# Optimization experiments

Hardware: AMD Instinct MI355X
Metric: run time of the kernel (lower is better)

The kernel has to match this reference:

```python
import jax, jax.numpy as jnp
import numpy as np

B, H, Q_TOK, D = 8, 12, 577, 64
N_SIDE = 24  # 24x24 = 576 patches, +1 CLS row/col -> 577


def _pairwise_dists():
    rows, cols = np.indices((N_SIDE, N_SIDE))
    idx = np.stack([rows.flatten(), cols.flatten()], axis=-1).astype(np.float32)  # (576, 2)
    d = idx[:, None, :] - idx[None, :, :]  # (576, 576, 2)
    d = np.pad(d, ((1, 0), (1, 0), (0, 0)))  # zero-pad CLS token row/col -> (577, 577, 2)
    return jnp.asarray(d)


def setup_inputs() -> dict:
    key = jax.random.key(0)
    ks = jax.random.split(key, 4)
    query = jax.random.normal(ks[0], (B, H, Q_TOK, D), jnp.float32)
    W1 = jax.random.normal(ks[1], (D, 64), jnp.float32) * 0.05
    b1 = jnp.zeros((64,), jnp.float32)
    W2 = jax.random.normal(ks[2], (64, 3), jnp.float32) * 0.05
    b2 = jnp.zeros((3,), jnp.float32)
    # uniform noise for RelaxedBernoulli reparameterized sample
    u = jax.random.uniform(ks[3], (B, H, Q_TOK, Q_TOK), jnp.float32, 1e-6, 1.0 - 1e-6)
    temperature = jnp.ones((1,), jnp.float32)
    return {"query": query, "W1": W1, "b1": b1, "W2": W2, "b2": b2,
            "dists": _pairwise_dists(), "u": u, "temperature": temperature}


def reference(query, W1, b1, W2, b2, dists, u, temperature):
    # sigma MLP: Linear -> exact GELU -> Linear, per (b,h,q) token
    hdn = jax.nn.gelu(query @ W1 + b1, approximate=False)
    sig = hdn @ W2 + b2  # (b,h,q,3)
    sy = jnp.exp(sig[..., 0]) + 1.0
    sx = jnp.exp(sig[..., 1]) + 1.0
    rho = jnp.tanh(sig[..., 2]) * 0.99
    cov = sy * sx * rho
    # 2x2 covariance matrix per query: [[sy^2, sy*sx*rho],[sy*sx*rho, sx^2]]
    Sigma = jnp.stack([jnp.stack([sy * sy, cov], -1),
                       jnp.stack([cov, sx * sx], -1)], -2)  # (b,h,q,2,2)
    # closed-form 2x2 inverse (same math as torch.linalg.inv)
    det = (sy * sx) ** 2 * (1.0 - rho * rho)
    inv00 = (sx * sx) / det
    inv11 = (sy * sy) / det
    inv01 = -cov / det
    dy = dists[..., 0]  # (q,k)
    dx = dists[..., 1]
    # Mahalanobis quadratic form, fused (no (b,h,q,k,2,2) intermediates)
    quad = (inv00[..., None] * (dy * dy)
            + 2.0 * inv01[..., None] * (dy * dx)
            + inv11[..., None] * (dx * dx))  # (b,h,q,k)
    kernel = jnp.exp(-0.5 * quad)
    probs = kernel / jnp.max(kernel, axis=-1, keepdims=True)
    probs = jnp.minimum(probs, 1.0)
    # RelaxedBernoulli rsample: sigmoid((logit(p) + logistic_noise) / T)
    logits = jnp.log(probs) - jnp.log1p(-probs)
    noise = jnp.log(u) - jnp.log1p(-u)
    mask = jax.nn.sigmoid((logits + noise) / temperature[0])
    return mask, Sigma
```

## Files before the change

kernel.cpp:

```cpp
#include <hip/hip_runtime.h>
#include <math.h>

constexpr int BB = 8, HH = 12, QT = 577, DD = 64;
constexpr int NTOK = BB * HH * QT;
constexpr long long MASK_ELEMS = (long long)NTOK * QT;
constexpr int NBH = BB * HH;
constexpr int WAVES_PER_BLOCK = 8;
constexpr int CHUNKS = NBH / WAVES_PER_BLOCK;

using f4 = __attribute__((ext_vector_type(4))) float;

__global__ __launch_bounds__(256)
void mlp_sigma(const float* __restrict__ query,
               const float* __restrict__ W1,
               const float* __restrict__ b1,
               const float* __restrict__ W2,
               const float* __restrict__ b2,
               f4* __restrict__ Sig)
{
    const int token = (blockIdx.x * 256 + threadIdx.x) >> 6;
    const int lane  = threadIdx.x & 63;
    if (token >= NTOK) return;

    const float qv = query[(size_t)token * DD + lane];
    float acc = b1[lane];
#pragma unroll
    for (int i = 0; i < DD; ++i)
        acc = fmaf(__shfl(qv, i), W1[i * DD + lane], acc);
    const float h = 0.5f * acc * (1.0f + erff(acc * 0.7071067811865476f));

    float p0 = h * W2[lane * 3 + 0];
    float p1 = h * W2[lane * 3 + 1];
    float p2 = h * W2[lane * 3 + 2];
#pragma unroll
    for (int off = 32; off > 0; off >>= 1) {
        p0 += __shfl_xor(p0, off);
        p1 += __shfl_xor(p1, off);
        p2 += __shfl_xor(p2, off);
    }
    if (lane == 0) {
        const float sy  = expf(p0 + b2[0]) + 1.0f;
        const float sx  = expf(p1 + b2[1]) + 1.0f;
        const float rho = tanhf(p2 + b2[2]) * 0.99f;
        const float cov = sy * sx * rho;
        f4 s; s.x = sy * sy; s.y = cov; s.z = cov; s.w = sx * sx;
        Sig[token] = s;
    }
}

template<bool T1>
__device__ __forceinline__ float mask_elem(float g0, float g1, float g2,
                                           float j0, float j1, float j2,
                                           float uv, float invT)
{
    const float hq = fmaxf(fmaf(j2, g2, fmaf(j1, g1, j0 * g0)), 0.0f);
    const float E  = __expf(hq);
    const float a  = E - 1.0f;
    if (T1)
        return __fdividef(uv, fmaf(a, 1.0f - uv, uv));
    const float rr = __fdividef(a * (1.0f - uv), uv);
    return __fdividef(1.0f, 1.0f + __expf(__logf(rr) * invT));
}

template<bool T1>
__device__ __forceinline__ void do_row(const f4* __restrict__ G4,
                                       const float* __restrict__ up,
                                       float* __restrict__ mp,
                                       const float* __restrict__ u,
                                       float* __restrict__ out,
                                       unsigned base, int h, int NV,
                                       const int* bc, int lane,
                                       float j0, float j1, float j2, float invT)
{
#pragma unroll
    for (int p = 0; p < 3; ++p) {
        const int idx = p * 64 + lane;
        if (idx < NV) {
            const f4 uu = *(const f4*)(up + 4 * idx);
            f4 m4;
#pragma unroll
            for (int c = 0; c < 4; ++c) {
                const f4 g = G4[bc[c] + idx];
                m4[c] = mask_elem<T1>(g.x, g.y, g.z, j0, j1, j2, uu[c], invT);
            }
            __builtin_nontemporal_store(m4, (f4*)(mp + 4 * idx));
        }
    }
    const int scnt = QT - 4 * NV;
    if (lane < scnt) {
        const int k = (lane < h) ? lane : (h + 4 * NV + (lane - h));
        const f4 g = G4[(k & 3) * 160 + (k >> 2)];
        const float m = mask_elem<T1>(g.x, g.y, g.z, j0, j1, j2,
                                      u[base + k], invT);
        __builtin_nontemporal_store(m, out + base + k);
    }
}

__global__ __launch_bounds__(512)
void mask_hyb(const float* __restrict__ u,
              const float* __restrict__ temp,
              float* __restrict__ out)
{
    __shared__ f4 G4[640];

    const f4* __restrict__ Sig = (const f4*)(out + MASK_ELEMS);
    const int q     = blockIdx.x;
    const int chunk = blockIdx.y;
    const int wave  = threadIdx.x >> 6;
    const int lane  = threadIdx.x & 63;

    const int token = (chunk * WAVES_PER_BLOCK + wave) * QT + q;
    const f4 S = Sig[token];
    const float tval = temp[0];

    const unsigned base = (unsigned)token * (unsigned)QT;
    const int h  = (int)((0u - base) & 3u);
    const int NV = (QT - h) >> 2;
    const float* __restrict__ up = u   + base + h;
    float*       __restrict__ mp = out + base + h;
    int bc[4];
#pragma unroll
    for (int c = 0; c < 4; ++c)
        bc[c] = ((h + c) & 3) * 160 + ((h + c) >> 2);

    {
        const int qm1 = (q > 0) ? q - 1 : 0;
        const int qr  = (int)((unsigned)qm1 / 24u);
        const int qc  = qm1 - qr * 24;
        const float fqr = (float)qr, fqc = (float)qc;
        const bool qz = (q == 0);
        for (int k = threadIdx.x; k < QT; k += 512) {
            const int km1 = (k > 0) ? k - 1 : 0;
            const int kr  = (int)((unsigned)km1 / 24u);
            const int kc  = km1 - kr * 24;
            float dy = fqr - (float)kr;
            float dx = fqc - (float)kc;
            if (qz | (k == 0)) { dy = 0.0f; dx = 0.0f; }
            f4 g; g.x = dy * dy; g.y = dy * dx; g.z = dx * dx; g.w = 0.0f;
            G4[(k & 3) * 160 + (k >> 2)] = g;
        }
    }
    __syncthreads();

    const float rdet = __fdividef(1.0f, fmaf(S.x, S.w, -S.y * S.y));
    const float j0 =  0.5f * S.w * rdet;
    const float j1 = -S.y * rdet;
    const float j2 =  0.5f * S.x * rdet;

    const float invT = __int_as_float(__builtin_amdgcn_readfirstlane(
                           __float_as_int(__fdividef(1.0f, tval))));
    if (invT == 1.0f)
        do_row<true >(G4, up, mp, u, out, base, h, NV, bc, lane, j0, j1, j2, invT);
    else
        do_row<false>(G4, up, mp, u, out, base, h, NV, bc, lane, j0, j1, j2, invT);
}

extern "C" void kernel_launch(void* const* d_in, const int* in_sizes, int n_in,
                              void* d_out, int out_size, void* d_ws, size_t ws_size,
                              hipStream_t stream) {
    const float* query = (const float*)d_in[0];
    const float* W1    = (const float*)d_in[1];
    const float* b1    = (const float*)d_in[2];
    const float* W2    = (const float*)d_in[3];
    const float* b2    = (const float*)d_in[4];
    const float* u     = (const float*)d_in[6];
    const float* temp  = (const float*)d_in[7];
    float* out = (float*)d_out;

    f4* Sig = (f4*)(out + MASK_ELEMS);
    mlp_sigma<<<dim3(NTOK / 4), dim3(256), 0, stream>>>(query, W1, b1, W2, b2, Sig);
    mask_hyb<<<dim3(QT, CHUNKS), dim3(512), 0, stream>>>(u, temp, out);
}
```

Measured before the change: 303.2 us.

## Fuse sigma MLP into mask kernel and prefetch u row before compute

Removes the separate MLP kernel and computes each token's sigma inside the mask kernel: W1 is staged in shared memory per block and each wave runs the 64x64 MLP for its own query token. The u row loads are issued up front so their latency overlaps the MLP and the distance-table setup. This drops one launch and the Sigma round-trip through global memory. In exchange, every block reloads W1 (16KB) into LDS, which raises shared-memory use and could lower occupancy.

```diff
diff --git a/kernel.cpp b/kernel.cpp
--- a/kernel.cpp
+++ b/kernel.cpp
@@ -9,44 +9,6 @@
 constexpr int CHUNKS = NBH / WAVES_PER_BLOCK;
 
 using f4 = __attribute__((ext_vector_type(4))) float;
-
-__global__ __launch_bounds__(256)
-void mlp_sigma(const float* __restrict__ query,
-               const float* __restrict__ W1,
-               const float* __restrict__ b1,
-               const float* __restrict__ W2,
-               const float* __restrict__ b2,
-               f4* __restrict__ Sig)
-{
-    const int token = (blockIdx.x * 256 + threadIdx.x) >> 6;
-    const int lane  = threadIdx.x & 63;
-    if (token >= NTOK) return;
-
-    const float qv = query[(size_t)token * DD + lane];
-    float acc = b1[lane];
-#pragma unroll
-    for (int i = 0; i < DD; ++i)
-        acc = fmaf(__shfl(qv, i), W1[i * DD + lane], acc);
-    const float h = 0.5f * acc * (1.0f + erff(acc * 0.7071067811865476f));
-
-    float p0 = h * W2[lane * 3 + 0];
-    float p1 = h * W2[lane * 3 + 1];
-    float p2 = h * W2[lane * 3 + 2];
-#pragma unroll
-    for (int off = 32; off > 0; off >>= 1) {
-        p0 += __shfl_xor(p0, off);
-        p1 += __shfl_xor(p1, off);
-        p2 += __shfl_xor(p2, off);
-    }
-    if (lane == 0) {
-        const float sy  = expf(p0 + b2[0]) + 1.0f;
-        const float sx  = expf(p1 + b2[1]) + 1.0f;
-        const float rho = tanhf(p2 + b2[2]) * 0.99f;
-        const float cov = sy * sx * rho;
-        f4 s; s.x = sy * sy; s.y = cov; s.z = cov; s.w = sx * sx;
-        Sig[token] = s;
-    }
-}
 
 template<bool T1>
 __device__ __forceinline__ float mask_elem(float g0, float g1, float g2,
@@ -63,65 +25,62 @@
 }
 
 template<bool T1>
-__device__ __forceinline__ void do_row(const f4* __restrict__ G4,
-                                       const float* __restrict__ up,
-                                       float* __restrict__ mp,
-                                       const float* __restrict__ u,
-                                       float* __restrict__ out,
-                                       unsigned base, int h, int NV,
-                                       const int* bc, int lane,
-                                       float j0, float j1, float j2, float invT)
+__device__ __forceinline__ void do_pass(const f4* __restrict__ G4,
+                                        const int* bc, int idx, f4 uu,
+                                        float* __restrict__ mp,
+                                        float j0, float j1, float j2, float invT)
 {
+    f4 m4;
 #pragma unroll
-    for (int p = 0; p < 3; ++p) {
-        const int idx = p * 64 + lane;
-        if (idx < NV) {
-            const f4 uu = *(const f4*)(up + 4 * idx);
-            f4 m4;
-#pragma unroll
-            for (int c = 0; c < 4; ++c) {
-                const f4 g = G4[bc[c] + idx];
-                m4[c] = mask_elem<T1>(g.x, g.y, g.z, j0, j1, j2, uu[c], invT);
-            }
-            __builtin_nontemporal_store(m4, (f4*)(mp + 4 * idx));
-        }
+    for (int c = 0; c < 4; ++c) {
+        const f4 g = G4[bc[c] + idx];
+        m4[c] = mask_elem<T1>(g.x, g.y, g.z, j0, j1, j2, uu[c], invT);
     }
-    const int scnt = QT - 4 * NV;
-    if (lane < scnt) {
-        const int k = (lane < h) ? lane : (h + 4 * NV + (lane - h));
-        const f4 g = G4[(k & 3) * 160 + (k >> 2)];
-        const float m = mask_elem<T1>(g.x, g.y, g.z, j0, j1, j2,
-                                      u[base + k], invT);
-        __builtin_nontemporal_store(m, out + base + k);
-    }
+    __builtin_nontemporal_store(m4, (f4*)(mp + 4 * idx));
 }
 
-__global__ __launch_bounds__(512)
-void mask_hyb(const float* __restrict__ u,
-              const float* __restrict__ temp,
-              float* __restrict__ out)
+__global__ __launch_bounds__(512, 6)
+void fused_mask(const float* __restrict__ query,
+                const float* __restrict__ W1,
+                const float* __restrict__ b1,
+                const float* __restrict__ W2,
+                const float* __restrict__ b2,
+                const float* __restrict__ u,
+                const float* __restrict__ temp,
+                float* __restrict__ out)
 {
-    __shared__ f4 G4[640];
+    __shared__ f4    G4[640];
+    __shared__ float W1s[DD * DD];
 
-    const f4* __restrict__ Sig = (const f4*)(out + MASK_ELEMS);
+    f4* __restrict__ SigOut = (f4*)(out + MASK_ELEMS);
     const int q     = blockIdx.x;
     const int chunk = blockIdx.y;
-    const int wave  = threadIdx.x >> 6;
-    const int lane  = threadIdx.x & 63;
+    const int tid   = threadIdx.x;
+    const int wave  = tid >> 6, lane = tid & 63;
 
     const int token = (chunk * WAVES_PER_BLOCK + wave) * QT + q;
-    const f4 S = Sig[token];
-    const float tval = temp[0];
-
     const unsigned base = (unsigned)token * (unsigned)QT;
     const int h  = (int)((0u - base) & 3u);
     const int NV = (QT - h) >> 2;
     const float* __restrict__ up = u   + base + h;
     float*       __restrict__ mp = out + base + h;
-    int bc[4];
-#pragma unroll
-    for (int c = 0; c < 4; ++c)
-        bc[c] = ((h + c) & 3) * 160 + ((h + c) >> 2);
+
+    const f4 uu0 = *(const f4*)(up + 4 * lane);
+    const f4 uu1 = *(const f4*)(up + 4 * (64 + lane));
+    const int idx2 = 128 + lane;
+    f4 uu2 = {};
+    if (idx2 < NV) uu2 = *(const f4*)(up + 4 * idx2);
+    const int scnt = QT - 4 * NV;
+    int ks = 0; float us = 0.0f;
+    if (lane < scnt) {
+        ks = (lane < h) ? lane : (h + 4 * NV + (lane - h));
+        us = u[base + ks];
+    }
+    const float tval = temp[0];
+    const float qv   = query[(size_t)token * DD + lane];
+
+    ((f4*)W1s)[tid]       = ((const f4*)W1)[tid];
+    ((f4*)W1s)[tid + 512] = ((const f4*)W1)[tid + 512];
 
     {
         const int qm1 = (q > 0) ? q - 1 : 0;
@@ -129,7 +88,7 @@
         const int qc  = qm1 - qr * 24;
         const float fqr = (float)qr, fqc = (float)qc;
         const bool qz = (q == 0);
-        for (int k = threadIdx.x; k < QT; k += 512) {
+        for (int k = tid; k < QT; k += 512) {
             const int km1 = (k > 0) ? k - 1 : 0;
             const int kr  = (int)((unsigned)km1 / 24u);
             const int kc  = km1 - kr * 24;
@@ -142,17 +101,64 @@
     }
     __syncthreads();
 
-    const float rdet = __fdividef(1.0f, fmaf(S.x, S.w, -S.y * S.y));
-    const float j0 =  0.5f * S.w * rdet;
-    const float j1 = -S.y * rdet;
-    const float j2 =  0.5f * S.x * rdet;
+    float acc = b1[lane];
+#pragma unroll
+    for (int i = 0; i < DD; ++i)
+        acc = fmaf(__shfl(qv, i), W1s[i * DD + lane], acc);
+    const float hg = 0.5f * acc * (1.0f + erff(acc * 0.7071067811865476f));
+
+    float p0 = hg * W2[lane * 3 + 0];
+    float p1 = hg * W2[lane * 3 + 1];
+    float p2 = hg * W2[lane * 3 + 2];
+#pragma unroll
+    for (int off = 32; off > 0; off >>= 1) {
+        p0 += __shfl_xor(p0, off);
+        p1 += __shfl_xor(p1, off);
+        p2 += __shfl_xor(p2, off);
+    }
+    const float sy  = expf(p0 + b2[0]) + 1.0f;
+    const float sx  = expf(p1 + b2[1]) + 1.0f;
+    const float rho = tanhf(p2 + b2[2]) * 0.99f;
+    const float cov = sy * sx * rho;
+    const float Sx = sy * sy, Sw = sx * sx, Sy = cov;
+    if (lane == 0) {
+        f4 s; s.x = Sx; s.y = Sy; s.z = Sy; s.w = Sw;
+        SigOut[token] = s;
+    }
+
+    const float rdet = __fdividef(1.0f, fmaf(Sx, Sw, -Sy * Sy));
+    const float j0 =  0.5f * Sw * rdet;
+    const float j1 = -Sy * rdet;
+    const float j2 =  0.5f * Sx * rdet;
+
+    int bc[4];
+#pragma unroll
+    for (int c = 0; c < 4; ++c)
+        bc[c] = ((h + c) & 3) * 160 + ((h + c) >> 2);
 
     const float invT = __int_as_float(__builtin_amdgcn_readfirstlane(
                            __float_as_int(__fdividef(1.0f, tval))));
-    if (invT == 1.0f)
-        do_row<true >(G4, up, mp, u, out, base, h, NV, bc, lane, j0, j1, j2, invT);
-    else
-        do_row<false>(G4, up, mp, u, out, base, h, NV, bc, lane, j0, j1, j2, invT);
+    if (invT == 1.0f) {
+        do_pass<true >(G4, bc, lane,      uu0, mp, j0, j1, j2, invT);
+        do_pass<true >(G4, bc, 64 + lane, uu1, mp, j0, j1, j2, invT);
+        if (idx2 < NV)
+            do_pass<true >(G4, bc, idx2,  uu2, mp, j0, j1, j2, invT);
+        if (lane < scnt) {
+            const f4 g = G4[(ks & 3) * 160 + (ks >> 2)];
+            const float m = mask_elem<true >(g.x, g.y, g.z, j0, j1, j2, us, invT);
+            __builtin_nontemporal_store(m, out + base + ks);
+        }
+    } else {
+        do_pass<false>(G4, bc, lane,      uu0, mp, j0, j1, j2, invT);
+        do_pass<false>(G4, bc, 64 + lane, uu1, mp, j0, j1, j2, invT);
+        if (idx2 < NV)
+            do_pass<false>(G4, bc, idx2,  uu2, mp, j0, j1, j2, invT);
+        if (lane < scnt) {
+            const f4 g = G4[(ks & 3) * 160 + (ks >> 2)];
+            const float m = mask_elem<false>(g.x, g.y, g.z, j0, j1, j2, us, invT);
+            __builtin_nontemporal_store(m, out + base + ks);
+        }
+    }
 }
 
 extern "C" void kernel_launch(void* const* d_in, const int* in_sizes, int n_in,
@@ -167,7 +173,6 @@
     const float* temp  = (const float*)d_in[7];
     float* out = (float*)d_out;
 
-    f4* Sig = (f4*)(out + MASK_ELEMS);
-    mlp_sigma<<<dim3(NTOK / 4), dim3(256), 0, stream>>>(query, W1, b1, W2, b2, Sig);
-    mask_hyb<<<dim3(QT, CHUNKS), dim3(512), 0, stream>>>(u, temp, out);
+    fused_mask<<<dim3(QT, CHUNKS), dim3(512), 0, stream>>>(
+        query, W1, b1, W2, b2, u, temp, out);
 }
```

Measured after the change: 265.2 us. 12.5% less time.
